# Performance work log

Hardware: AMD Instinct MI355X
Metric: run time of the kernel (lower is better)

Reference implementation:

```python
import jax, jax.numpy as jnp
import numpy as np

B, N_OBJ, OBJ_D = 256, 36, 2048
ATT_D, EMB_D, DEC_D, VOCAB, T = 1024, 1024, 1024, 10000, 20


def setup_inputs() -> dict:
    key = jax.random.key(0)
    ks = jax.random.split(key, 16)
    s = lambda *d: 1.0 / np.sqrt(d[-1])
    inp = {
        'encoder_out': jax.random.normal(ks[0], (B, EMB_D), jnp.float32),
        'objects': jax.random.normal(ks[1], (B, N_OBJ, OBJ_D), jnp.float32),
        'encoded_captions': jax.random.randint(ks[2], (B, T), 0, VOCAB),
        'caption_lengths': jax.random.randint(ks[3], (B, 1), 1, T + 1),
        'emb_table': jax.random.normal(ks[4], (VOCAB, EMB_D), jnp.float32) * 0.02,
        'W_enc_att': jax.random.normal(ks[5], (ATT_D, OBJ_D), jnp.float32) * s(OBJ_D),
        'b_enc_att': jnp.zeros((ATT_D,), jnp.float32),
        'W_dec_att': jax.random.normal(ks[6], (ATT_D, DEC_D), jnp.float32) * s(DEC_D),
        'b_dec_att': jnp.zeros((ATT_D,), jnp.float32),
        'w_full_att': jax.random.normal(ks[7], (1, ATT_D), jnp.float32) * s(ATT_D),
        'b_full_att': jnp.zeros((1,), jnp.float32),
        'W_fbeta': jax.random.normal(ks[8], (OBJ_D, DEC_D), jnp.float32) * s(DEC_D),
        'b_fbeta': jnp.zeros((OBJ_D,), jnp.float32),
        'W_ih': jax.random.normal(ks[9], (4 * DEC_D, EMB_D + OBJ_D), jnp.float32) * s(EMB_D + OBJ_D),
        'W_hh': jax.random.normal(ks[10], (4 * DEC_D, DEC_D), jnp.float32) * s(DEC_D),
        'b_ih': jnp.zeros((4 * DEC_D,), jnp.float32),
        'b_hh': jnp.zeros((4 * DEC_D,), jnp.float32),
        'W_fc': jax.random.normal(ks[11], (VOCAB, DEC_D), jnp.float32) * s(DEC_D),
        'b_fc': jnp.zeros((VOCAB,), jnp.float32),
    }
    return inp


def reference(encoder_out, objects, encoded_captions, caption_lengths,
              emb_table, W_enc_att, b_enc_att, W_dec_att, b_dec_att,
              w_full_att, b_full_att, W_fbeta, b_fbeta,
              W_ih, W_hh, b_ih, b_hh, W_fc, b_fc):
    lengths = caption_lengths[:, 0]
    sort_ind = jnp.argsort(-lengths)  # descending
    lengths = lengths[sort_ind]
    encoder_out = encoder_out[sort_ind]
    objects = objects[sort_ind]
    encoded_captions = encoded_captions[sort_ind]

    embeddings = emb_table[encoded_captions]  # (B, T, E)
    # step t input: encoder_out at t=0, embeddings[:, t-1] afterwards
    step_x = jnp.concatenate([encoder_out[:, None, :], embeddings[:, : T - 1, :]], axis=1)  # (B,T,E)

    att1 = jnp.einsum('bno,ao->bna', objects, W_enc_att) + b_enc_att  # (B,N,A), h-independent

    def step(carry, xs):
        h, c = carry
        x_t, t = xs  # (B,E), scalar
        active = (t < lengths)[:, None]  # (B,1) -- batch_size_t masking (lengths sorted desc)
        att2 = h @ W_dec_att.T + b_dec_att  # (B,A)
        e = (jax.nn.relu(att1 + att2[:, None, :]) @ w_full_att[0] + b_full_att[0])  # (B,N)
        alpha = jax.nn.softmax(e, axis=1)
        awe = jnp.einsum('bn,bno->bo', alpha, objects)  # (B,O)
        gate = jax.nn.sigmoid(h @ W_fbeta.T + b_fbeta)
        awe = gate * awe
        gates = jnp.concatenate([x_t, awe], axis=-1) @ W_ih.T + b_ih + h @ W_hh.T + b_hh
        i, f, g, o = jnp.split(gates, 4, axis=-1)  # torch LSTMCell order
        c_new = jax.nn.sigmoid(f) * c + jax.nn.sigmoid(i) * jnp.tanh(g)
        h_new = jax.nn.sigmoid(o) * jnp.tanh(c_new)
        h = jnp.where(active, h_new, h)
        c = jnp.where(active, c_new, c)
        preds = h_new @ W_fc.T + b_fc  # dropout in eval mode = identity
        preds = jnp.where(active, preds, 0.0)
        alpha = jnp.where(active, alpha, 0.0)
        return (h, c), (preds, alpha)

    h0 = jnp.zeros((B, DEC_D), objects.dtype)
    c0 = jnp.zeros((B, DEC_D), objects.dtype)
    xs = (jnp.swapaxes(step_x, 0, 1), jnp.arange(T))
    _, (preds, alphas) = jax.lax.scan(step, (h0, c0), xs)
    predictions = jnp.swapaxes(preds, 0, 1)  # (B,T,V)
    alphas = jnp.swapaxes(alphas, 0, 1)      # (B,T,N)
    return predictions, encoded_captions, lengths, alphas, sort_ind
```

## Files before the change

kernel.cpp:

```cpp
#include <hip/hip_runtime.h>
#include <hip/hip_bf16.h>
#include <cstdint>
#include <cstddef>

#define BB 256
#define TT 20
#define NOBJ 36
#define OBJD 2048
#define ATTD 1024
#define DECD 1024
#define VOCAB 10000
#define NBIG  17168
#define NBIGP 17280
#define NSPLIT 7168

typedef unsigned short u16;
typedef __attribute__((ext_vector_type(8))) short short8v;
typedef __attribute__((ext_vector_type(4))) float float4v;

__device__ inline u16 f2bf(float f) {
    __hip_bfloat16 h = __float2bfloat16(f);
    return *reinterpret_cast<u16*>(&h);
}
__device__ inline float bu(u16 u) {
    union { unsigned int i; float f; } x;
    x.i = ((unsigned int)u) << 16;
    return x.f;
}
__device__ inline float sigf(float x) { return 1.f / (1.f + expf(-x)); }

__device__ inline void gload16(const u16* g, u16* l) {
    __builtin_amdgcn_global_load_lds(
        (const __attribute__((address_space(1))) unsigned int*)g,
        (__attribute__((address_space(3))) unsigned int*)l, 16, 0, 0);
}

__global__ __launch_bounds__(256) void sort_kernel(
    const int* __restrict__ lens, int* __restrict__ sidx, int* __restrict__ slen,
    int* __restrict__ cnt, float* __restrict__ out_len, float* __restrict__ out_sind)
{
    __shared__ int L[BB];
    __shared__ int SL[BB];
    const int i = threadIdx.x;
    const int li = lens[i];
    L[i] = li;
    __syncthreads();
    int r = 0;
    for (int j = 0; j < BB; ++j) {
        const int lj = L[j];
        if (lj > li || (lj == li && j < i)) r++;
    }
    sidx[r] = i;
    slen[r] = li;
    SL[r] = li;
    out_sind[r] = (float)i;
    out_len[r]  = (float)li;
    __syncthreads();
    if (i < TT) {
        int cc = 0;
        for (int b = 0; b < BB; ++b) cc += (SL[b] > i);
        cnt[i] = cc;
    }
}

__global__ __launch_bounds__(256) void meta_kernel(
    const int* __restrict__ caps, const int* __restrict__ sidx,
    float* __restrict__ out_caps)
{
    const int idx = blockIdx.x * 256 + threadIdx.x;
    const int p = idx / TT, t = idx % TT;
    out_caps[idx] = (float)caps[sidx[p] * TT + t];
}

__global__ __launch_bounds__(256) void gather_objs(
    const float* __restrict__ objs, const int* __restrict__ sidx,
    u16* __restrict__ objsb)
{
    const int row = blockIdx.x;
    const int b = row / NOBJ, n = row - b * NOBJ;
    const float* src = objs + ((size_t)sidx[b] * NOBJ + n) * OBJD;
    u16* dst = objsb + (size_t)row * OBJD;
    const int tid = threadIdx.x;
    #pragma unroll
    for (int j = 0; j < 2; ++j) {
        float4 v = ((const float4*)src)[tid + 256 * j];
        ushort4 s;
        s.x = f2bf(v.x); s.y = f2bf(v.y); s.z = f2bf(v.z); s.w = f2bf(v.w);
        ((ushort4*)dst)[tid + 256 * j] = s;
    }
}

__global__ __launch_bounds__(256) void convWbig(
    const float* __restrict__ Wda, const float* __restrict__ bda,
    const float* __restrict__ Wfb, const float* __restrict__ bfb,
    const float* __restrict__ Whh,
    const float* __restrict__ Wfc, const float* __restrict__ bfc,
    u16* __restrict__ Wb, float* __restrict__ bcat)
{
    const int n = blockIdx.x;
    const int tid = threadIdx.x;
    const float* src = nullptr;
    float bb = 0.f;
    if (n < 1024)        { src = Wda + (size_t)n * 1024;            bb = bda[n]; }
    else if (n < 3072)   { src = Wfb + (size_t)(n - 1024) * 1024;   bb = bfb[n - 1024]; }
    else if (n < 7168)   { src = Whh + (size_t)(n - 3072) * 1024;   bb = 0.f; }
    else if (n < NBIG)   { src = Wfc + (size_t)(n - 7168) * 1024;   bb = bfc[n - 7168]; }
    u16* dst = Wb + (size_t)n * 1024;
    ushort4 s;
    if (src) {
        float4 v = ((const float4*)src)[tid];
        s.x = f2bf(v.x); s.y = f2bf(v.y); s.z = f2bf(v.z); s.w = f2bf(v.w);
    } else { s.x = s.y = s.z = s.w = 0; }
    ((ushort4*)dst)[tid] = s;
    if (tid == 0) bcat[n] = bb;
}

__global__ __launch_bounds__(256) void convWih(
    const float* __restrict__ Wih, const float* __restrict__ bih,
    const float* __restrict__ bhh, u16* __restrict__ Wb, float* __restrict__ bsum)
{
    const int n = blockIdx.x;
    const int tid = threadIdx.x;
    const float* src = Wih + (size_t)n * 3072;
    u16* dst = Wb + (size_t)n * 3072;
    #pragma unroll
    for (int j = 0; j < 3; ++j) {
        float4 v = ((const float4*)src)[tid + 256 * j];
        ushort4 s;
        s.x = f2bf(v.x); s.y = f2bf(v.y); s.z = f2bf(v.z); s.w = f2bf(v.w);
        ((ushort4*)dst)[tid + 256 * j] = s;
    }
    if (tid == 0) bsum[n] = bih[n] + bhh[n];
}

__global__ __launch_bounds__(256) void convWea(
    const float* __restrict__ Wea, u16* __restrict__ Wb)
{
    const int n = blockIdx.x;
    const int tid = threadIdx.x;
    const float* src = Wea + (size_t)n * OBJD;
    u16* dst = Wb + (size_t)n * OBJD;
    #pragma unroll
    for (int j = 0; j < 2; ++j) {
        float4 v = ((const float4*)src)[tid + 256 * j];
        ushort4 s;
        s.x = f2bf(v.x); s.y = f2bf(v.y); s.z = f2bf(v.z); s.w = f2bf(v.w);
        ((ushort4*)dst)[tid + 256 * j] = s;
    }
}

__global__ __launch_bounds__(256) void embed_kernel(
    const float* __restrict__ enc, const int* __restrict__ caps,
    const float* __restrict__ emb, const int* __restrict__ sidx,
    u16* __restrict__ Xb)
{
    const int blk = blockIdx.x;
    const int t = blk >> 8;
    const int b = blk & 255;
    const int sb = sidx[b];
    const float* src = (t == 0) ? (enc + (size_t)sb * DECD)
                                : (emb + (size_t)caps[sb * TT + (t - 1)] * DECD);
    const int tid = threadIdx.x;
    float4 v = ((const float4*)src)[tid];
    ushort4 s;
    s.x = f2bf(v.x); s.y = f2bf(v.y); s.z = f2bf(v.z); s.w = f2bf(v.w);
    ((ushort4*)(Xb + (size_t)blk * DECD))[tid] = s;
}

__global__ __launch_bounds__(256) void zero_hc(float* __restrict__ h, float* __restrict__ c)
{
    const int idx = blockIdx.x * 256 + threadIdx.x;
    if (idx < BB * DECD) h[idx] = 0.f;
    else                 c[idx - BB * DECD] = 0.f;
}

__global__ __launch_bounds__(256) void hcat0_kernel(
    const float* __restrict__ bcat, float* __restrict__ Hcat)
{
    const int col4 = blockIdx.x * 256 + threadIdx.x;
    const int m = blockIdx.y;
    ((float4*)(Hcat + (size_t)m * 7168))[col4] = ((const float4*)bcat)[col4];
}

__global__ __launch_bounds__(256) void gemm128(
    const u16* __restrict__ A, int lda,
    const u16* __restrict__ B, int ldb,
    const float* __restrict__ bias,
    float* __restrict__ Cf, u16* __restrict__ Cb, int ldc,
    int Nreal, int kzlen, size_t zCstride, int pairM,
    int nsplit, float* __restrict__ C2, int ldc2, const int* __restrict__ cntp)
{
    __shared__ u16 As[3][128 * 32];
    __shared__ u16 Bs[3][128 * 32];
    const int tid = threadIdx.x;
    const int lane = tid & 63;
    const int w = tid >> 6;
    const int wr = w >> 1, wc = w & 1;
    int nIdx, mIdx;
    if (pairM) { nIdx = blockIdx.x >> 1; mIdx = blockIdx.x & 1; }
    else       { nIdx = blockIdx.x;      mIdx = blockIdx.y; }
    const int m0 = mIdx * 128;
    const int n0 = nIdx * 128;
    const int kbase = blockIdx.z * kzlen;
    A += kbase;
    B += kbase;
    if (Cf) Cf += (size_t)blockIdx.z * zCstride;

    const int act = cntp ? *cntp : (1 << 30);
    float4v acc[4][4];
    #pragma unroll
    for (int i = 0; i < 4; ++i)
        #pragma unroll
        for (int j = 0; j < 4; ++j) acc[i][j] = (float4v){0.f, 0.f, 0.f, 0.f};

    if (m0 < act) {
        const int r0 = (w * 2 + 0) * 16 + (lane >> 2);
        const int r1 = (w * 2 + 1) * 16 + (lane >> 2);
        const int s0 = (lane & 3) ^ ((r0 >> 1) & 3);
        const int s1 = (lane & 3) ^ ((r1 >> 1) & 3);
        const u16* gA0 = A + (size_t)(m0 + r0) * lda + s0 * 8;
        const u16* gA1 = A + (size_t)(m0 + r1) * lda + s1 * 8;
        const u16* gB0 = B + (size_t)(n0 + r0) * ldb + s0 * 8;
        const u16* gB1 = B + (size_t)(n0 + r1) * ldb + s1 * 8;
        const int la0 = (w * 2 + 0) * 16 * 32;
        const int la1 = (w * 2 + 1) * 16 * 32;

        int ia[4], ib[4];
        #pragma unroll
        for (int mi = 0; mi < 4; ++mi) {
            const int r = wr * 64 + mi * 16 + (lane & 15);
            ia[mi] = r * 32 + (((lane >> 4) ^ ((r >> 1) & 3)) << 3);
        }
        #pragma unroll
        for (int nj = 0; nj < 4; ++nj) {
            const int r = wc * 64 + nj * 16 + (lane & 15);
            ib[nj] = r * 32 + (((lane >> 4) ^ ((r >> 1) & 3)) << 3);
        }

        const int nk = kzlen >> 5;
        #pragma unroll
        for (int p = 0; p < 3; ++p) {
            if (p < nk) {
                const int ko = p * 32;
                gload16(gA0 + ko, &As[p][la0]);
                gload16(gA1 + ko, &As[p][la1]);
                gload16(gB0 + ko, &Bs[p][la0]);
                gload16(gB1 + ko, &Bs[p][la1]);
            }
        }
        int cur = 0;
        for (int it = 0; it < nk; ++it) {
            const int rem = nk - 1 - it;
            if (rem >= 2)      asm volatile("s_waitcnt vmcnt(8)" ::: "memory");
            else if (rem == 1) asm volatile("s_waitcnt vmcnt(4)" ::: "memory");
            else               asm volatile("s_waitcnt vmcnt(0)" ::: "memory");
            __builtin_amdgcn_s_barrier();
            short8v av[4], bv[4];
            #pragma unroll
            for (int mi = 0; mi < 4; ++mi) av[mi] = *(const short8v*)&As[cur][ia[mi]];
            #pragma unroll
            for (int nj = 0; nj < 4; ++nj) bv[nj] = *(const short8v*)&Bs[cur][ib[nj]];
            __builtin_amdgcn_s_setprio(1);
            #pragma unroll
            for (int mi = 0; mi < 4; ++mi)
                #pragma unroll
                for (int nj = 0; nj < 4; ++nj)
                    acc[mi][nj] = __builtin_amdgcn_mfma_f32_16x16x32_bf16(
                        av[mi], bv[nj], acc[mi][nj], 0, 0, 0);
            __builtin_amdgcn_s_setprio(0);
            __builtin_amdgcn_s_barrier();
            if (it + 3 < nk) {
                const int ko = (it + 3) * 32;
                gload16(gA0 + ko, &As[cur][la0]);
                gload16(gA1 + ko, &As[cur][la1]);
                gload16(gB0 + ko, &Bs[cur][la0]);
                gload16(gB1 + ko, &Bs[cur][la1]);
            }
            cur = (cur == 2) ? 0 : cur + 1;
        }
    }

    #pragma unroll
    for (int mi = 0; mi < 4; ++mi) {
        const int mbase = m0 + wr * 64 + mi * 16 + ((lane >> 4) << 2);
        #pragma unroll
        for (int nj = 0; nj < 4; ++nj) {
            const int n = n0 + wc * 64 + nj * 16 + (lane & 15);
            if (n >= Nreal) continue;
            const float bval = bias ? bias[n] : 0.f;
            #pragma unroll
            for (int r = 0; r < 4; ++r) {
                const int m = mbase + r;
                const float v = acc[mi][nj][r] + bval;
                if (n < nsplit) {
                    if (Cb) Cb[(size_t)m * ldc + n] = f2bf(v);
                    else    Cf[(size_t)m * ldc + n] = v;
                } else {
                    C2[(size_t)m * ldc2 + (n - nsplit)] = (m < act) ? v : 0.f;
                }
            }
        }
    }
}

__global__ __launch_bounds__(256) void attn_kernel(
    const u16* __restrict__ att1b, const float* __restrict__ Hcat,
    const u16* __restrict__ objsb,
    const float* __restrict__ wfa, const float* __restrict__ bfa,
    const int* __restrict__ slen, int t,
    float* __restrict__ out_alph, u16* __restrict__ aweb)
{
    const int b = blockIdx.x, z = blockIdx.y, tid = threadIdx.x;
    const bool active = t < slen[b];
    if (!active) {
        if (z == 0 && tid < NOBJ)
            out_alph[((size_t)b * TT + t) * NOBJ + tid] = 0.f;
        return;
    }
    __shared__ float wred[4][40];
    __shared__ float es[40];
    __shared__ float alph[40];
    const int lane = tid & 63, w = tid >> 6;
    const float* hrow = Hcat + (size_t)b * 7168;
    const float4 h4 = ((const float4*)hrow)[tid];
    const float4 w4 = ((const float4*)wfa)[tid];
    const u16* a1base = att1b + (size_t)b * NOBJ * ATTD;

    float ep[NOBJ];
    #pragma unroll
    for (int n = 0; n < NOBJ; ++n) {
        ushort4 a4 = ((const ushort4*)(a1base + (size_t)n * ATTD))[tid];
        const float v0 = fmaxf(bu(a4.x) + h4.x, 0.f);
        const float v1 = fmaxf(bu(a4.y) + h4.y, 0.f);
        const float v2 = fmaxf(bu(a4.z) + h4.z, 0.f);
        const float v3 = fmaxf(bu(a4.w) + h4.w, 0.f);
        ep[n] = v0 * w4.x + v1 * w4.y + v2 * w4.z + v3 * w4.w;
    }
    #pragma unroll
    for (int n = 0; n < NOBJ; ++n) {
        float p = ep[n];
        #pragma unroll
        for (int off = 32; off > 0; off >>= 1) p += __shfl_down(p, off, 64);
        if (lane == 0) wred[w][n] = p;
    }
    __syncthreads();
    if (tid < NOBJ)
        es[tid] = wred[0][tid] + wred[1][tid] + wred[2][tid] + wred[3][tid] + bfa[0];
    __syncthreads();
    if (tid < 64) {
        float mv = (tid < NOBJ) ? es[tid] : -1e30f;
        #pragma unroll
        for (int off = 32; off > 0; off >>= 1) mv = fmaxf(mv, __shfl_xor(mv, off, 64));
        float e = (tid < NOBJ) ? expf(es[tid] - mv) : 0.f;
        float s = e;
        #pragma unroll
        for (int off = 32; off > 0; off >>= 1) s += __shfl_xor(s, off, 64);
        if (tid < NOBJ) alph[tid] = e / s;
    }
    __syncthreads();
    if (z == 0 && tid < NOBJ)
        out_alph[((size_t)b * TT + t) * NOBJ + tid] = alph[tid];

    float acc[4] = {0.f, 0.f, 0.f, 0.f};
    const u16* ob = objsb + (size_t)b * NOBJ * OBJD + z * 1024 + tid * 4;
    #pragma unroll 4
    for (int n = 0; n < NOBJ; ++n) {
        const ushort4 ov = *(const ushort4*)(ob + (size_t)n * OBJD);
        const float al = alph[n];
        acc[0] = fmaf(al, bu(ov.x), acc[0]);
        acc[1] = fmaf(al, bu(ov.y), acc[1]);
        acc[2] = fmaf(al, bu(ov.z), acc[2]);
        acc[3] = fmaf(al, bu(ov.w), acc[3]);
    }
    const float4 g0 = *(const float4*)(hrow + 1024 + z * 1024 + tid * 4);
    ushort4 st;
    st.x = f2bf(acc[0] * sigf(g0.x));
    st.y = f2bf(acc[1] * sigf(g0.y));
    st.z = f2bf(acc[2] * sigf(g0.z));
    st.w = f2bf(acc[3] * sigf(g0.w));
    *(ushort4*)&aweb[(size_t)b * 2048 + z * 1024 + tid * 4] = st;
}

__global__ __launch_bounds__(256) void lstm_kernel(
    const float* __restrict__ G2p, const u16* __restrict__ Gxb,
    const float* __restrict__ Hcat,
    float* __restrict__ h, float* __restrict__ c, u16* __restrict__ hb,
    const int* __restrict__ slen, int t)
{
    const int idx = blockIdx.x * 256 + threadIdx.x;
    const int b = idx >> 8, d4 = idx & 255;
    if (t >= slen[b]) return;
    const float4* pw = (const float4*)(Hcat + (size_t)b * 7168 + 3072);
    const u16* gx = Gxb + ((size_t)(t * BB + b)) * 4096;

    float4 g[4];
    #pragma unroll
    for (int q = 0; q < 4; ++q) {
        const ushort4 xv = ((const ushort4*)(gx + q * 1024))[d4];
        float4 s;
        s.x = bu(xv.x); s.y = bu(xv.y); s.z = bu(xv.z); s.w = bu(xv.w);
        const float4 hv = pw[q * 256 + d4];
        s.x += hv.x; s.y += hv.y; s.z += hv.z; s.w += hv.w;
        #pragma unroll
        for (int p = 0; p < 4; ++p) {
            const float4 pv = ((const float4*)G2p)[(size_t)p * (BB * 1024) + b * 1024 + q * 256 + d4];
            s.x += pv.x; s.y += pv.y; s.z += pv.z; s.w += pv.w;
        }
        g[q] = s;
    }
    float4* hp = (float4*)(h + (size_t)b * 1024);
    float4* cp = (float4*)(c + (size_t)b * 1024);
    const float4 cold = cp[d4];
    float4 cn, hn;
    {
        const float si = sigf(g[0].x), sf = sigf(g[1].x), so = sigf(g[3].x);
        cn.x = sf * cold.x + si * tanhf(g[2].x); hn.x = so * tanhf(cn.x);
    }
    {
        const float si = sigf(g[0].y), sf = sigf(g[1].y), so = sigf(g[3].y);
        cn.y = sf * cold.y + si * tanhf(g[2].y); hn.y = so * tanhf(cn.y);
    }
    {
        const float si = sigf(g[0].z), sf = sigf(g[1].z), so = sigf(g[3].z);
        cn.z = sf * cold.z + si * tanhf(g[2].z); hn.z = so * tanhf(cn.z);
    }
    {
        const float si = sigf(g[0].w), sf = sigf(g[1].w), so = sigf(g[3].w);
        cn.w = sf * cold.w + si * tanhf(g[2].w); hn.w = so * tanhf(cn.w);
    }
    hp[d4] = hn;
    cp[d4] = cn;
    ushort4 s;
    s.x = f2bf(hn.x); s.y = f2bf(hn.y); s.z = f2bf(hn.z); s.w = f2bf(hn.w);
    ((ushort4*)(hb + (size_t)b * 1024))[d4] = s;
}

extern "C" void kernel_launch(void* const* d_in, const int* in_sizes, int n_in,
                              void* d_out, int out_size, void* d_ws, size_t ws_size,
                              hipStream_t stream)
{
    const float* enc  = (const float*)d_in[0];
    const float* objs = (const float*)d_in[1];
    const int*   caps = (const int*)d_in[2];
    const int*   clen = (const int*)d_in[3];
    const float* emb  = (const float*)d_in[4];
    const float* Wea  = (const float*)d_in[5];
    const float* bea  = (const float*)d_in[6];
    const float* Wda  = (const float*)d_in[7];
    const float* bda  = (const float*)d_in[8];
    const float* wfa  = (const float*)d_in[9];
    const float* bfa  = (const float*)d_in[10];
    const float* Wfb  = (const float*)d_in[11];
    const float* bfb  = (const float*)d_in[12];
    const float* Wih  = (const float*)d_in[13];
    const float* Whh  = (const float*)d_in[14];
    const float* bih  = (const float*)d_in[15];
    const float* bhh  = (const float*)d_in[16];
    const float* Wfc  = (const float*)d_in[17];
    const float* bfc  = (const float*)d_in[18];

    float* outP     = (float*)d_out;
    float* out_caps = outP + (size_t)BB * TT * VOCAB;
    float* out_len  = out_caps + BB * TT;
    float* out_alph = out_len + BB;
    float* out_sind = out_alph + (size_t)BB * TT * NOBJ;

    char* wp = (char*)d_ws;
    auto alloc = [&](size_t bytes) -> void* {
        void* r = (void*)wp;
        wp += (bytes + 255) & ~(size_t)255;
        return r;
    };
    int*   sidx  = (int*)alloc(BB * 4);
    int*   slen  = (int*)alloc(BB * 4);
    int*   cnt   = (int*)alloc(32 * 4);
    u16*   objsb = (u16*)alloc((size_t)BB * NOBJ * OBJD * 2);
    u16*   Wbigb = (u16*)alloc((size_t)NBIGP * 1024 * 2);
    float* bcat  = (float*)alloc(NBIGP * 4);
    u16*   Wihb  = (u16*)alloc((size_t)4096 * 3072 * 2);
    float* bsum  = (float*)alloc(4096 * 4);
    u16*   Weab  = (u16*)alloc((size_t)1024 * OBJD * 2);
    u16*   att1b = (u16*)alloc((size_t)BB * NOBJ * ATTD * 2);
    u16*   Xb    = (u16*)alloc((size_t)TT * BB * DECD * 2);
    u16*   Gxb   = (u16*)alloc((size_t)TT * BB * 4096 * 2);
    float* Hcat  = (float*)alloc((size_t)BB * 7168 * 4);
    u16*   aweb  = (u16*)alloc((size_t)BB * 2048 * 2);
    float* G2p   = (float*)alloc((size_t)4 * BB * 4096 * 4);
    float* h     = (float*)alloc((size_t)BB * DECD * 4);
    float* c     = (float*)alloc((size_t)BB * DECD * 4);
    u16*   hb    = (u16*)alloc((size_t)BB * DECD * 2);
    (void)ws_size; (void)in_sizes; (void)n_in; (void)out_size;

    sort_kernel<<<1, 256, 0, stream>>>(clen, sidx, slen, cnt, out_len, out_sind);
    meta_kernel<<<20, 256, 0, stream>>>(caps, sidx, out_caps);
    gather_objs<<<BB * NOBJ, 256, 0, stream>>>(objs, sidx, objsb);
    convWbig<<<NBIGP, 256, 0, stream>>>(Wda, bda, Wfb, bfb, Whh, Wfc, bfc, Wbigb, bcat);
    convWih<<<4096, 256, 0, stream>>>(Wih, bih, bhh, Wihb, bsum);
    convWea<<<1024, 256, 0, stream>>>(Wea, Weab);
    embed_kernel<<<TT * BB, 256, 0, stream>>>(enc, caps, emb, sidx, Xb);
    zero_hc<<<2048, 256, 0, stream>>>(h, c);
    hcat0_kernel<<<dim3(7, 256), 256, 0, stream>>>(bcat, Hcat);

    gemm128<<<dim3(8, 72, 1), 256, 0, stream>>>(
        objsb, OBJD, Weab, OBJD, bea, nullptr, att1b, ATTD,
        ATTD, OBJD, 0, 0, 1 << 30, nullptr, 0, nullptr);

    gemm128<<<dim3(32, 40, 1), 256, 0, stream>>>(
        Xb, DECD, Wihb, 3072, bsum, nullptr, Gxb, 4096,
        4096, DECD, 0, 0, 1 << 30, nullptr, 0, nullptr);

    for (int t = 0; t < TT; ++t) {
        attn_kernel<<<dim3(BB, 2), 256, 0, stream>>>(
            att1b, Hcat, objsb, wfa, bfa, slen, t, out_alph, aweb);
        gemm128<<<dim3(64, 1, 4), 256, 0, stream>>>(
            aweb, 2048, Wihb + 1024, 3072, nullptr, G2p, nullptr, 4096,
            4096, 512, (size_t)BB * 4096, 1, 1 << 30, nullptr, 0, cnt + t);
        lstm_kernel<<<256, 256, 0, stream>>>(G2p, Gxb, Hcat, h, c, hb, slen, t);
        gemm128<<<dim3(NBIGP / 64, 1, 1), 256, 0, stream>>>(
            hb, DECD, Wbigb, DECD, bcat, Hcat, nullptr, 7168,
            NBIG, DECD, 0, 1, NSPLIT, outP + (size_t)t * VOCAB, TT * VOCAB, cnt + t);
    }
}
```

Before: 1.704 ms.

## Fuse all stages into one persistent megakernel with software grid barriers

Replaces the separate preprocessing, GEMM, attention and LSTM launches with a single persistent kernel of 256 blocks that steps through the phases and synchronises them with an atomic grid barrier. The goal is to remove the many per-timestep kernel launches and the idle gaps between them. GEMM tiles are now handed out as a job loop. Only the M tiles needed for the active batch rows are scheduled, and the attention job processes the full 2048-wide object row per block. The trade-off is one block per CU for the heavy prologue GEMMs, which may lower latency hiding, plus barrier spin costs and the risk of deadlock if not all blocks are co-resident.

```diff
diff --git a/kernel.cpp b/kernel.cpp
--- a/kernel.cpp
+++ b/kernel.cpp
@@ -13,6 +13,7 @@
 #define NBIG  17168
 #define NBIGP 17280
 #define NSPLIT 7168
+#define NGRID 256
 
 typedef unsigned short u16;
 typedef __attribute__((ext_vector_type(8))) short short8v;
@@ -35,185 +36,60 @@
         (__attribute__((address_space(3))) unsigned int*)l, 16, 0, 0);
 }
 
-__global__ __launch_bounds__(256) void sort_kernel(
-    const int* __restrict__ lens, int* __restrict__ sidx, int* __restrict__ slen,
-    int* __restrict__ cnt, float* __restrict__ out_len, float* __restrict__ out_sind)
-{
-    __shared__ int L[BB];
-    __shared__ int SL[BB];
-    const int i = threadIdx.x;
-    const int li = lens[i];
-    L[i] = li;
+struct MegaParams {
+    const float* enc; const float* objs; const int* caps; const int* clen;
+    const float* emb;
+    const float* Wea; const float* bea; const float* Wda; const float* bda;
+    const float* wfa; const float* bfa; const float* Wfb; const float* bfb;
+    const float* Wih; const float* Whh; const float* bih; const float* bhh;
+    const float* Wfc; const float* bfc;
+    float* outP; float* out_caps; float* out_len; float* out_alph; float* out_sind;
+    int* bar; int* sidx; int* slen; int* cnt;
+    u16* objsb; u16* Wbigb; float* bcat; u16* Wihb; float* bsum; u16* Weab;
+    u16* att1b; u16* Xb; u16* Gxb; float* Hcat; u16* aweb; float* G2p;
+    float* h; float* c; u16* hb;
+};
+
+__device__ inline void grid_bar(int* bar) {
     __syncthreads();
-    int r = 0;
-    for (int j = 0; j < BB; ++j) {
-        const int lj = L[j];
-        if (lj > li || (lj == li && j < i)) r++;
-    }
-    sidx[r] = i;
-    slen[r] = li;
-    SL[r] = li;
-    out_sind[r] = (float)i;
-    out_len[r]  = (float)li;
+    if (threadIdx.x == 0) {
+        __threadfence();
+        const int gen = __hip_atomic_load(&bar[1], __ATOMIC_RELAXED, __HIP_MEMORY_SCOPE_AGENT);
+        const int prev = __hip_atomic_fetch_add(&bar[0], 1, __ATOMIC_ACQ_REL, __HIP_MEMORY_SCOPE_AGENT);
+        if (prev == NGRID - 1) {
+            __hip_atomic_store(&bar[0], 0, __ATOMIC_RELAXED, __HIP_MEMORY_SCOPE_AGENT);
+            __hip_atomic_store(&bar[1], gen + 1, __ATOMIC_RELEASE, __HIP_MEMORY_SCOPE_AGENT);
+        } else {
+            while (__hip_atomic_load(&bar[1], __ATOMIC_RELAXED, __HIP_MEMORY_SCOPE_AGENT) == gen) {
+                __builtin_amdgcn_s_sleep(1);
+            }
+        }
+        __threadfence();
+    }
     __syncthreads();
-    if (i < TT) {
-        int cc = 0;
-        for (int b = 0; b < BB; ++b) cc += (SL[b] > i);
-        cnt[i] = cc;
-    }
-}
-
-__global__ __launch_bounds__(256) void meta_kernel(
-    const int* __restrict__ caps, const int* __restrict__ sidx,
-    float* __restrict__ out_caps)
-{
-    const int idx = blockIdx.x * 256 + threadIdx.x;
-    const int p = idx / TT, t = idx % TT;
-    out_caps[idx] = (float)caps[sidx[p] * TT + t];
-}
-
-__global__ __launch_bounds__(256) void gather_objs(
-    const float* __restrict__ objs, const int* __restrict__ sidx,
-    u16* __restrict__ objsb)
-{
-    const int row = blockIdx.x;
-    const int b = row / NOBJ, n = row - b * NOBJ;
-    const float* src = objs + ((size_t)sidx[b] * NOBJ + n) * OBJD;
-    u16* dst = objsb + (size_t)row * OBJD;
-    const int tid = threadIdx.x;
-    #pragma unroll
-    for (int j = 0; j < 2; ++j) {
-        float4 v = ((const float4*)src)[tid + 256 * j];
-        ushort4 s;
-        s.x = f2bf(v.x); s.y = f2bf(v.y); s.z = f2bf(v.z); s.w = f2bf(v.w);
-        ((ushort4*)dst)[tid + 256 * j] = s;
-    }
-}
-
-__global__ __launch_bounds__(256) void convWbig(
-    const float* __restrict__ Wda, const float* __restrict__ bda,
-    const float* __restrict__ Wfb, const float* __restrict__ bfb,
-    const float* __restrict__ Whh,
-    const float* __restrict__ Wfc, const float* __restrict__ bfc,
-    u16* __restrict__ Wb, float* __restrict__ bcat)
-{
-    const int n = blockIdx.x;
-    const int tid = threadIdx.x;
-    const float* src = nullptr;
-    float bb = 0.f;
-    if (n < 1024)        { src = Wda + (size_t)n * 1024;            bb = bda[n]; }
-    else if (n < 3072)   { src = Wfb + (size_t)(n - 1024) * 1024;   bb = bfb[n - 1024]; }
-    else if (n < 7168)   { src = Whh + (size_t)(n - 3072) * 1024;   bb = 0.f; }
-    else if (n < NBIG)   { src = Wfc + (size_t)(n - 7168) * 1024;   bb = bfc[n - 7168]; }
-    u16* dst = Wb + (size_t)n * 1024;
-    ushort4 s;
-    if (src) {
-        float4 v = ((const float4*)src)[tid];
-        s.x = f2bf(v.x); s.y = f2bf(v.y); s.z = f2bf(v.z); s.w = f2bf(v.w);
-    } else { s.x = s.y = s.z = s.w = 0; }
-    ((ushort4*)dst)[tid] = s;
-    if (tid == 0) bcat[n] = bb;
-}
-
-__global__ __launch_bounds__(256) void convWih(
-    const float* __restrict__ Wih, const float* __restrict__ bih,
-    const float* __restrict__ bhh, u16* __restrict__ Wb, float* __restrict__ bsum)
-{
-    const int n = blockIdx.x;
-    const int tid = threadIdx.x;
-    const float* src = Wih + (size_t)n * 3072;
-    u16* dst = Wb + (size_t)n * 3072;
-    #pragma unroll
-    for (int j = 0; j < 3; ++j) {
-        float4 v = ((const float4*)src)[tid + 256 * j];
-        ushort4 s;
-        s.x = f2bf(v.x); s.y = f2bf(v.y); s.z = f2bf(v.z); s.w = f2bf(v.w);
-        ((ushort4*)dst)[tid + 256 * j] = s;
-    }
-    if (tid == 0) bsum[n] = bih[n] + bhh[n];
-}
-
-__global__ __launch_bounds__(256) void convWea(
-    const float* __restrict__ Wea, u16* __restrict__ Wb)
-{
-    const int n = blockIdx.x;
-    const int tid = threadIdx.x;
-    const float* src = Wea + (size_t)n * OBJD;
-    u16* dst = Wb + (size_t)n * OBJD;
-    #pragma unroll
-    for (int j = 0; j < 2; ++j) {
-        float4 v = ((const float4*)src)[tid + 256 * j];
-        ushort4 s;
-        s.x = f2bf(v.x); s.y = f2bf(v.y); s.z = f2bf(v.z); s.w = f2bf(v.w);
-        ((ushort4*)dst)[tid + 256 * j] = s;
-    }
-}
-
-__global__ __launch_bounds__(256) void embed_kernel(
-    const float* __restrict__ enc, const int* __restrict__ caps,
-    const float* __restrict__ emb, const int* __restrict__ sidx,
-    u16* __restrict__ Xb)
-{
-    const int blk = blockIdx.x;
-    const int t = blk >> 8;
-    const int b = blk & 255;
-    const int sb = sidx[b];
-    const float* src = (t == 0) ? (enc + (size_t)sb * DECD)
-                                : (emb + (size_t)caps[sb * TT + (t - 1)] * DECD);
-    const int tid = threadIdx.x;
-    float4 v = ((const float4*)src)[tid];
-    ushort4 s;
-    s.x = f2bf(v.x); s.y = f2bf(v.y); s.z = f2bf(v.z); s.w = f2bf(v.w);
-    ((ushort4*)(Xb + (size_t)blk * DECD))[tid] = s;
-}
-
-__global__ __launch_bounds__(256) void zero_hc(float* __restrict__ h, float* __restrict__ c)
-{
-    const int idx = blockIdx.x * 256 + threadIdx.x;
-    if (idx < BB * DECD) h[idx] = 0.f;
-    else                 c[idx - BB * DECD] = 0.f;
-}
-
-__global__ __launch_bounds__(256) void hcat0_kernel(
-    const float* __restrict__ bcat, float* __restrict__ Hcat)
-{
-    const int col4 = blockIdx.x * 256 + threadIdx.x;
-    const int m = blockIdx.y;
-    ((float4*)(Hcat + (size_t)m * 7168))[col4] = ((const float4*)bcat)[col4];
-}
-
-__global__ __launch_bounds__(256) void gemm128(
+}
+
+__device__ void gemm_job(
+    u16* AsB, u16* BsB,
     const u16* __restrict__ A, int lda,
     const u16* __restrict__ B, int ldb,
     const float* __restrict__ bias,
-    float* __restrict__ Cf, u16* __restrict__ Cb, int ldc,
-    int Nreal, int kzlen, size_t zCstride, int pairM,
-    int nsplit, float* __restrict__ C2, int ldc2, const int* __restrict__ cntp)
+    float* Cf, u16* Cb, int ldc,
+    int Nreal, int K, int m0, int n0,
+    int nsplit, float* C2, int ldc2, int act)
 {
-    __shared__ u16 As[3][128 * 32];
-    __shared__ u16 Bs[3][128 * 32];
     const int tid = threadIdx.x;
     const int lane = tid & 63;
     const int w = tid >> 6;
     const int wr = w >> 1, wc = w & 1;
-    int nIdx, mIdx;
-    if (pairM) { nIdx = blockIdx.x >> 1; mIdx = blockIdx.x & 1; }
-    else       { nIdx = blockIdx.x;      mIdx = blockIdx.y; }
-    const int m0 = mIdx * 128;
-    const int n0 = nIdx * 128;
-    const int kbase = blockIdx.z * kzlen;
-    A += kbase;
-    B += kbase;
-    if (Cf) Cf += (size_t)blockIdx.z * zCstride;
-
-    const int act = cntp ? *cntp : (1 << 30);
+
     float4v acc[4][4];
     #pragma unroll
     for (int i = 0; i < 4; ++i)
         #pragma unroll
         for (int j = 0; j < 4; ++j) acc[i][j] = (float4v){0.f, 0.f, 0.f, 0.f};
 
-    if (m0 < act) {
+    {
         const int r0 = (w * 2 + 0) * 16 + (lane >> 2);
         const int r1 = (w * 2 + 1) * 16 + (lane >> 2);
         const int s0 = (lane & 3) ^ ((r0 >> 1) & 3);
@@ -222,8 +98,8 @@
         const u16* gA1 = A + (size_t)(m0 + r1) * lda + s1 * 8;
         const u16* gB0 = B + (size_t)(n0 + r0) * ldb + s0 * 8;
         const u16* gB1 = B + (size_t)(n0 + r1) * ldb + s1 * 8;
-        const int la0 = (w * 2 + 0) * 16 * 32;
-        const int la1 = (w * 2 + 1) * 16 * 32;
+        const int la0 = (w * 2 + 0) * 512;
+        const int la1 = (w * 2 + 1) * 512;
 
         int ia[4], ib[4];
         #pragma unroll
@@ -237,16 +113,14 @@
             ib[nj] = r * 32 + (((lane >> 4) ^ ((r >> 1) & 3)) << 3);
         }
 
-        const int nk = kzlen >> 5;
+        const int nk = K >> 5;
         #pragma unroll
         for (int p = 0; p < 3; ++p) {
-            if (p < nk) {
-                const int ko = p * 32;
-                gload16(gA0 + ko, &As[p][la0]);
-                gload16(gA1 + ko, &As[p][la1]);
-                gload16(gB0 + ko, &Bs[p][la0]);
-                gload16(gB1 + ko, &Bs[p][la1]);
-            }
+            const int ko = p * 32;
+            gload16(gA0 + ko, AsB + p * 4096 + la0);
+            gload16(gA1 + ko, AsB + p * 4096 + la1);
+            gload16(gB0 + ko, BsB + p * 4096 + la0);
+            gload16(gB1 + ko, BsB + p * 4096 + la1);
         }
         int cur = 0;
         for (int it = 0; it < nk; ++it) {
@@ -255,11 +129,13 @@
             else if (rem == 1) asm volatile("s_waitcnt vmcnt(4)" ::: "memory");
             else               asm volatile("s_waitcnt vmcnt(0)" ::: "memory");
             __builtin_amdgcn_s_barrier();
+            const u16* Asc = AsB + cur * 4096;
+            const u16* Bsc = BsB + cur * 4096;
             short8v av[4], bv[4];
             #pragma unroll
-            for (int mi = 0; mi < 4; ++mi) av[mi] = *(const short8v*)&As[cur][ia[mi]];
+            for (int mi = 0; mi < 4; ++mi) av[mi] = *(const short8v*)&Asc[ia[mi]];
             #pragma unroll
-            for (int nj = 0; nj < 4; ++nj) bv[nj] = *(const short8v*)&Bs[cur][ib[nj]];
+            for (int nj = 0; nj < 4; ++nj) bv[nj] = *(const short8v*)&Bsc[ib[nj]];
             __builtin_amdgcn_s_setprio(1);
             #pragma unroll
             for (int mi = 0; mi < 4; ++mi)
@@ -271,10 +147,12 @@
             __builtin_amdgcn_s_barrier();
             if (it + 3 < nk) {
                 const int ko = (it + 3) * 32;
-                gload16(gA0 + ko, &As[cur][la0]);
-                gload16(gA1 + ko, &As[cur][la1]);
-                gload16(gB0 + ko, &Bs[cur][la0]);
-                gload16(gB1 + ko, &Bs[cur][la1]);
+                u16* Asw = AsB + cur * 4096;
+                u16* Bsw = BsB + cur * 4096;
+                gload16(gA0 + ko, Asw + la0);
+                gload16(gA1 + ko, Asw + la1);
+                gload16(gB0 + ko, Bsw + la0);
+                gload16(gB1 + ko, Bsw + la1);
             }
             cur = (cur == 2) ? 0 : cur + 1;
         }
@@ -295,36 +173,24 @@
                 if (n < nsplit) {
                     if (Cb) Cb[(size_t)m * ldc + n] = f2bf(v);
                     else    Cf[(size_t)m * ldc + n] = v;
-                } else {
-                    C2[(size_t)m * ldc2 + (n - nsplit)] = (m < act) ? v : 0.f;
+                } else if (m < act) {
+                    C2[(size_t)m * ldc2 + (n - nsplit)] = v;
                 }
             }
         }
     }
 }
 
-__global__ __launch_bounds__(256) void attn_kernel(
-    const u16* __restrict__ att1b, const float* __restrict__ Hcat,
-    const u16* __restrict__ objsb,
-    const float* __restrict__ wfa, const float* __restrict__ bfa,
-    const int* __restrict__ slen, int t,
-    float* __restrict__ out_alph, u16* __restrict__ aweb)
+__device__ void attn_job(const MegaParams& P, int b, int t,
+                         float (*wred)[40], float* es, float* alph)
 {
-    const int b = blockIdx.x, z = blockIdx.y, tid = threadIdx.x;
-    const bool active = t < slen[b];
-    if (!active) {
-        if (z == 0 && tid < NOBJ)
-            out_alph[((size_t)b * TT + t) * NOBJ + tid] = 0.f;
-        return;
-    }
-    __shared__ float wred[4][40];
-    __shared__ float es[40];
-    __shared__ float alph[40];
+    const int tid = threadIdx.x;
+    if (t >= P.slen[b]) return;
     const int lane = tid & 63, w = tid >> 6;
-    const float* hrow = Hcat + (size_t)b * 7168;
+    const float* hrow = P.Hcat + (size_t)b * 7168;
     const float4 h4 = ((const float4*)hrow)[tid];
-    const float4 w4 = ((const float4*)wfa)[tid];
-    const u16* a1base = att1b + (size_t)b * NOBJ * ATTD;
+    const float4 w4 = ((const float4*)P.wfa)[tid];
+    const u16* a1base = P.att1b + (size_t)b * NOBJ * ATTD;
 
     float ep[NOBJ];
     #pragma unroll
@@ -345,7 +211,7 @@
     }
     __syncthreads();
     if (tid < NOBJ)
-        es[tid] = wred[0][tid] + wred[1][tid] + wred[2][tid] + wred[3][tid] + bfa[0];
+        es[tid] = wred[0][tid] + wred[1][tid] + wred[2][tid] + wred[3][tid] + P.bfa[0];
     __syncthreads();
     if (tid < 64) {
         float mv = (tid < NOBJ) ? es[tid] : -1e30f;
@@ -358,40 +224,35 @@
         if (tid < NOBJ) alph[tid] = e / s;
     }
     __syncthreads();
-    if (z == 0 && tid < NOBJ)
-        out_alph[((size_t)b * TT + t) * NOBJ + tid] = alph[tid];
-
-    float acc[4] = {0.f, 0.f, 0.f, 0.f};
-    const u16* ob = objsb + (size_t)b * NOBJ * OBJD + z * 1024 + tid * 4;
+    if (tid < NOBJ)
+        P.out_alph[((size_t)b * TT + t) * NOBJ + tid] = alph[tid];
+
+    float acc[8] = {0.f, 0.f, 0.f, 0.f, 0.f, 0.f, 0.f, 0.f};
+    const u16* ob = P.objsb + (size_t)b * NOBJ * OBJD + tid * 8;
     #pragma unroll 4
     for (int n = 0; n < NOBJ; ++n) {
-        const ushort4 ov = *(const ushort4*)(ob + (size_t)n * OBJD);
+        const short8v ov = *(const short8v*)(ob + (size_t)n * OBJD);
         const float al = alph[n];
-        acc[0] = fmaf(al, bu(ov.x), acc[0]);
-        acc[1] = fmaf(al, bu(ov.y), acc[1]);
-        acc[2] = fmaf(al, bu(ov.z), acc[2]);
-        acc[3] = fmaf(al, bu(ov.w), acc[3]);
-    }
-    const float4 g0 = *(const float4*)(hrow + 1024 + z * 1024 + tid * 4);
-    ushort4 st;
-    st.x = f2bf(acc[0] * sigf(g0.x));
-    st.y = f2bf(acc[1] * sigf(g0.y));
-    st.z = f2bf(acc[2] * sigf(g0.z));
-    st.w = f2bf(acc[3] * sigf(g0.w));
-    *(ushort4*)&aweb[(size_t)b * 2048 + z * 1024 + tid * 4] = st;
-}
-
-__global__ __launch_bounds__(256) void lstm_kernel(
-    const float* __restrict__ G2p, const u16* __restrict__ Gxb,
-    const float* __restrict__ Hcat,
-    float* __restrict__ h, float* __restrict__ c, u16* __restrict__ hb,
-    const int* __restrict__ slen, int t)
+        #pragma unroll
+        for (int j = 0; j < 8; ++j) acc[j] = fmaf(al, bu((u16)ov[j]), acc[j]);
+    }
+    const float* gp = hrow + 1024 + tid * 8;
+    const float4 g0 = *(const float4*)gp;
+    const float4 g1 = *(const float4*)(gp + 4);
+    const float gt[8] = {sigf(g0.x), sigf(g0.y), sigf(g0.z), sigf(g0.w),
+                         sigf(g1.x), sigf(g1.y), sigf(g1.z), sigf(g1.w)};
+    short8v st;
+    #pragma unroll
+    for (int j = 0; j < 8; ++j) st[j] = (short)f2bf(acc[j] * gt[j]);
+    *(short8v*)&P.aweb[(size_t)b * 2048 + tid * 8] = st;
+}
+
+__device__ void lstm_job(const MegaParams& P, int b, int t)
 {
-    const int idx = blockIdx.x * 256 + threadIdx.x;
-    const int b = idx >> 8, d4 = idx & 255;
-    if (t >= slen[b]) return;
-    const float4* pw = (const float4*)(Hcat + (size_t)b * 7168 + 3072);
-    const u16* gx = Gxb + ((size_t)(t * BB + b)) * 4096;
+    if (t >= P.slen[b]) return;
+    const int d4 = threadIdx.x;
+    const float4* pw = (const float4*)(P.Hcat + (size_t)b * 7168 + 3072);
+    const u16* gx = P.Gxb + ((size_t)(t * BB + b)) * 4096;
 
     float4 g[4];
     #pragma unroll
@@ -403,13 +264,13 @@
         s.x += hv.x; s.y += hv.y; s.z += hv.z; s.w += hv.w;
         #pragma unroll
         for (int p = 0; p < 4; ++p) {
-            const float4 pv = ((const float4*)G2p)[(size_t)p * (BB * 1024) + b * 1024 + q * 256 + d4];
+            const float4 pv = ((const float4*)P.G2p)[(size_t)p * (BB * 1024) + b * 1024 + q * 256 + d4];
             s.x += pv.x; s.y += pv.y; s.z += pv.z; s.w += pv.w;
         }
         g[q] = s;
     }
-    float4* hp = (float4*)(h + (size_t)b * 1024);
-    float4* cp = (float4*)(c + (size_t)b * 1024);
+    float4* hp = (float4*)(P.h + (size_t)b * 1024);
+    float4* cp = (float4*)(P.c + (size_t)b * 1024);
     const float4 cold = cp[d4];
     float4 cn, hn;
     {
@@ -432,38 +293,201 @@
     cp[d4] = cn;
     ushort4 s;
     s.x = f2bf(hn.x); s.y = f2bf(hn.y); s.z = f2bf(hn.z); s.w = f2bf(hn.w);
-    ((ushort4*)(hb + (size_t)b * 1024))[d4] = s;
+    ((ushort4*)(P.hb + (size_t)b * 1024))[d4] = s;
+}
+
+__global__ __launch_bounds__(256) void mega(MegaParams P)
+{
+    __shared__ u16 ldsA[3 * 4096];
+    __shared__ u16 ldsB[3 * 4096];
+    __shared__ float wred[4][40];
+    __shared__ float es[40];
+    __shared__ float alph[40];
+    __shared__ int Ls[BB];
+    __shared__ int SLs[BB];
+    const int bid = blockIdx.x;
+    const int tid = threadIdx.x;
+
+    if (bid == 0) {
+        const int li = P.clen[tid];
+        Ls[tid] = li;
+        __syncthreads();
+        int r = 0;
+        for (int j = 0; j < BB; ++j) {
+            const int lj = Ls[j];
+            if (lj > li || (lj == li && j < tid)) r++;
+        }
+        P.sidx[r] = tid; P.slen[r] = li; SLs[r] = li;
+        P.out_sind[r] = (float)tid; P.out_len[r] = (float)li;
+        __syncthreads();
+        if (tid < TT) {
+            int cc = 0;
+            for (int b2 = 0; b2 < BB; ++b2) cc += (SLs[b2] > tid);
+            P.cnt[tid] = cc;
+        }
+    }
+    for (int n = bid; n < NBIGP; n += NGRID) {
+        const float* src = nullptr;
+        float bbv = 0.f;
+        if (n < 1024)      { src = P.Wda + (size_t)n * 1024;          bbv = P.bda[n]; }
+        else if (n < 3072) { src = P.Wfb + (size_t)(n - 1024) * 1024; bbv = P.bfb[n - 1024]; }
+        else if (n < 7168) { src = P.Whh + (size_t)(n - 3072) * 1024; }
+        else if (n < NBIG) { src = P.Wfc + (size_t)(n - 7168) * 1024; bbv = P.bfc[n - 7168]; }
+        ushort4 s4;
+        if (src) {
+            float4 v = ((const float4*)src)[tid];
+            s4.x = f2bf(v.x); s4.y = f2bf(v.y); s4.z = f2bf(v.z); s4.w = f2bf(v.w);
+        } else { s4.x = s4.y = s4.z = s4.w = 0; }
+        ((ushort4*)(P.Wbigb + (size_t)n * 1024))[tid] = s4;
+        if (tid == 0) P.bcat[n] = bbv;
+    }
+    for (int n = bid; n < 4096; n += NGRID) {
+        const float* src = P.Wih + (size_t)n * 3072;
+        u16* dst = P.Wihb + (size_t)n * 3072;
+        #pragma unroll
+        for (int j = 0; j < 3; ++j) {
+            float4 v = ((const float4*)src)[tid + 256 * j];
+            ushort4 s4;
+            s4.x = f2bf(v.x); s4.y = f2bf(v.y); s4.z = f2bf(v.z); s4.w = f2bf(v.w);
+            ((ushort4*)dst)[tid + 256 * j] = s4;
+        }
+        if (tid == 0) P.bsum[n] = P.bih[n] + P.bhh[n];
+    }
+    for (int n = bid; n < 1024; n += NGRID) {
+        const float* src = P.Wea + (size_t)n * OBJD;
+        u16* dst = P.Weab + (size_t)n * OBJD;
+        #pragma unroll
+        for (int j = 0; j < 2; ++j) {
+            float4 v = ((const float4*)src)[tid + 256 * j];
+            ushort4 s4;
+            s4.x = f2bf(v.x); s4.y = f2bf(v.y); s4.z = f2bf(v.z); s4.w = f2bf(v.w);
+            ((ushort4*)dst)[tid + 256 * j] = s4;
+        }
+    }
+    {
+        const float4 z4 = make_float4(0.f, 0.f, 0.f, 0.f);
+        ((float4*)(P.h + (size_t)bid * 1024))[tid] = z4;
+        ((float4*)(P.c + (size_t)bid * 1024))[tid] = z4;
+        float4* o4 = (float4*)P.outP;
+        for (size_t i = (size_t)bid * 256 + tid; i < 12800000u; i += NGRID * 256) o4[i] = z4;
+        float4* a4 = (float4*)P.out_alph;
+        for (int i = bid * 256 + tid; i < 46080; i += NGRID * 256) a4[i] = z4;
+    }
+    grid_bar(P.bar);
+
+    for (int row = bid; row < BB * NOBJ; row += NGRID) {
+        const int b = row / NOBJ, n = row - b * NOBJ;
+        const float* src = P.objs + ((size_t)P.sidx[b] * NOBJ + n) * OBJD;
+        u16* dst = P.objsb + (size_t)row * OBJD;
+        #pragma unroll
+        for (int j = 0; j < 2; ++j) {
+            float4 v = ((const float4*)src)[tid + 256 * j];
+            ushort4 s4;
+            s4.x = f2bf(v.x); s4.y = f2bf(v.y); s4.z = f2bf(v.z); s4.w = f2bf(v.w);
+            ((ushort4*)dst)[tid + 256 * j] = s4;
+        }
+    }
+    for (int blk = bid; blk < TT * BB; blk += NGRID) {
+        const int t = blk >> 8, b = blk & 255;
+        const int sb = P.sidx[b];
+        const float* src = (t == 0) ? (P.enc + (size_t)sb * DECD)
+                                    : (P.emb + (size_t)P.caps[sb * TT + (t - 1)] * DECD);
+        float4 v = ((const float4*)src)[tid];
+        ushort4 s4;
+        s4.x = f2bf(v.x); s4.y = f2bf(v.y); s4.z = f2bf(v.z); s4.w = f2bf(v.w);
+        ((ushort4*)(P.Xb + (size_t)blk * DECD))[tid] = s4;
+    }
+    if (bid == 1) {
+        for (int i = tid; i < BB * TT; i += 256) {
+            const int p = i / TT, t = i % TT;
+            P.out_caps[i] = (float)P.caps[P.sidx[p] * TT + t];
+        }
+    }
+    {
+        const float4* src = (const float4*)P.bcat;
+        float4* dst = (float4*)(P.Hcat + (size_t)bid * 7168);
+        for (int i = tid; i < 1792; i += 256) dst[i] = src[i];
+    }
+    grid_bar(P.bar);
+
+    for (int j = bid; j < 576 + 1280; j += NGRID) {
+        if (j < 576) {
+            const int n = j / 72, m = j % 72;
+            gemm_job(ldsA, ldsB, P.objsb, OBJD, P.Weab, OBJD, P.bea,
+                     nullptr, P.att1b, ATTD, ATTD, OBJD, m * 128, n * 128,
+                     1 << 30, nullptr, 0, 1 << 30);
+        } else {
+            const int j2 = j - 576;
+            const int n = j2 / 40, m = j2 % 40;
+            gemm_job(ldsA, ldsB, P.Xb, DECD, P.Wihb, 3072, P.bsum,
+                     nullptr, P.Gxb, 4096, 4096, DECD, m * 128, n * 128,
+                     1 << 30, nullptr, 0, 1 << 30);
+        }
+    }
+    grid_bar(P.bar);
+
+    for (int t = 0; t < TT; ++t) {
+        const int act = P.cnt[t];
+        const int mt = (act > 128) ? 2 : 1;
+
+        attn_job(P, bid, t, wred, es, alph);
+        grid_bar(P.bar);
+
+        for (int j = bid; j < mt * 128; j += NGRID) {
+            const int kz = j & 3, q = j >> 2;
+            const int n = q & 31, m = q >> 5;
+            gemm_job(ldsA, ldsB,
+                     P.aweb + kz * 512, 2048,
+                     P.Wihb + 1024 + kz * 512, 3072,
+                     nullptr, P.G2p + (size_t)kz * (BB * 4096), nullptr, 4096,
+                     4096, 512, m * 128, n * 128, 1 << 30, nullptr, 0, 1 << 30);
+        }
+        grid_bar(P.bar);
+
+        lstm_job(P, bid, t);
+        grid_bar(P.bar);
+
+        for (int j = bid; j < mt * 135; j += NGRID) {
+            int n, m;
+            if (mt == 2) { n = j >> 1; m = j & 1; } else { n = j; m = 0; }
+            gemm_job(ldsA, ldsB, P.hb, DECD, P.Wbigb, DECD, P.bcat,
+                     P.Hcat, nullptr, 7168, NBIG, DECD, m * 128, n * 128,
+                     NSPLIT, P.outP + (size_t)t * VOCAB, TT * VOCAB, act);
+        }
+        grid_bar(P.bar);
+    }
 }
 
 extern "C" void kernel_launch(void* const* d_in, const int* in_sizes, int n_in,
                               void* d_out, int out_size, void* d_ws, size_t ws_size,
                               hipStream_t stream)
 {
-    const float* enc  = (const float*)d_in[0];
-    const float* objs = (const float*)d_in[1];
-    const int*   caps = (const int*)d_in[2];
-    const int*   clen = (const int*)d_in[3];
-    const float* emb  = (const float*)d_in[4];
-    const float* Wea  = (const float*)d_in[5];
-    const float* bea  = (const float*)d_in[6];
-    const float* Wda  = (const float*)d_in[7];
-    const float* bda  = (const float*)d_in[8];
-    const float* wfa  = (const float*)d_in[9];
-    const float* bfa  = (const float*)d_in[10];
-    const float* Wfb  = (const float*)d_in[11];
-    const float* bfb  = (const float*)d_in[12];
-    const float* Wih  = (const float*)d_in[13];
-    const float* Whh  = (const float*)d_in[14];
-    const float* bih  = (const float*)d_in[15];
-    const float* bhh  = (const float*)d_in[16];
-    const float* Wfc  = (const float*)d_in[17];
-    const float* bfc  = (const float*)d_in[18];
-
-    float* outP     = (float*)d_out;
-    float* out_caps = outP + (size_t)BB * TT * VOCAB;
-    float* out_len  = out_caps + BB * TT;
-    float* out_alph = out_len + BB;
-    float* out_sind = out_alph + (size_t)BB * TT * NOBJ;
+    MegaParams P;
+    P.enc  = (const float*)d_in[0];
+    P.objs = (const float*)d_in[1];
+    P.caps = (const int*)d_in[2];
+    P.clen = (const int*)d_in[3];
+    P.emb  = (const float*)d_in[4];
+    P.Wea  = (const float*)d_in[5];
+    P.bea  = (const float*)d_in[6];
+    P.Wda  = (const float*)d_in[7];
+    P.bda  = (const float*)d_in[8];
+    P.wfa  = (const float*)d_in[9];
+    P.bfa  = (const float*)d_in[10];
+    P.Wfb  = (const float*)d_in[11];
+    P.bfb  = (const float*)d_in[12];
+    P.Wih  = (const float*)d_in[13];
+    P.Whh  = (const float*)d_in[14];
+    P.bih  = (const float*)d_in[15];
+    P.bhh  = (const float*)d_in[16];
+    P.Wfc  = (const float*)d_in[17];
+    P.bfc  = (const float*)d_in[18];
+
+    P.outP     = (float*)d_out;
+    P.out_caps = P.outP + (size_t)BB * TT * VOCAB;
+    P.out_len  = P.out_caps + BB * TT;
+    P.out_alph = P.out_len + BB;
+    P.out_sind = P.out_alph + (size_t)BB * TT * NOBJ;
 
     char* wp = (char*)d_ws;
     auto alloc = [&](size_t bytes) -> void* {
@@ -471,53 +495,27 @@
         wp += (bytes + 255) & ~(size_t)255;
         return r;
     };
-    int*   sidx  = (int*)alloc(BB * 4);
-    int*   slen  = (int*)alloc(BB * 4);
-    int*   cnt   = (int*)alloc(32 * 4);
-    u16*   objsb = (u16*)alloc((size_t)BB * NOBJ * OBJD * 2);
-    u16*   Wbigb = (u16*)alloc((size_t)NBIGP * 1024 * 2);
-    float* bcat  = (float*)alloc(NBIGP * 4);
-    u16*   Wihb  = (u16*)alloc((size_t)4096 * 3072 * 2);
-    float* bsum  = (float*)alloc(4096 * 4);
-    u16*   Weab  = (u16*)alloc((size_t)1024 * OBJD * 2);
-    u16*   att1b = (u16*)alloc((size_t)BB * NOBJ * ATTD * 2);
-    u16*   Xb    = (u16*)alloc((size_t)TT * BB * DECD * 2);
-    u16*   Gxb   = (u16*)alloc((size_t)TT * BB * 4096 * 2);
-    float* Hcat  = (float*)alloc((size_t)BB * 7168 * 4);
-    u16*   aweb  = (u16*)alloc((size_t)BB * 2048 * 2);
-    float* G2p   = (float*)alloc((size_t)4 * BB * 4096 * 4);
-    float* h     = (float*)alloc((size_t)BB * DECD * 4);
-    float* c     = (float*)alloc((size_t)BB * DECD * 4);
-    u16*   hb    = (u16*)alloc((size_t)BB * DECD * 2);
+    P.bar   = (int*)alloc(256);
+    P.sidx  = (int*)alloc(BB * 4);
+    P.slen  = (int*)alloc(BB * 4);
+    P.cnt   = (int*)alloc(32 * 4);
+    P.objsb = (u16*)alloc((size_t)BB * NOBJ * OBJD * 2);
+    P.Wbigb = (u16*)alloc((size_t)NBIGP * 1024 * 2);
+    P.bcat  = (float*)alloc(NBIGP * 4);
+    P.Wihb  = (u16*)alloc((size_t)4096 * 3072 * 2);
+    P.bsum  = (float*)alloc(4096 * 4);
+    P.Weab  = (u16*)alloc((size_t)1024 * OBJD * 2);
+    P.att1b = (u16*)alloc((size_t)BB * NOBJ * ATTD * 2);
+    P.Xb    = (u16*)alloc((size_t)TT * BB * DECD * 2);
+    P.Gxb   = (u16*)alloc((size_t)TT * BB * 4096 * 2);
+    P.Hcat  = (float*)alloc((size_t)BB * 7168 * 4);
+    P.aweb  = (u16*)alloc((size_t)BB * 2048 * 2);
+    P.G2p   = (float*)alloc((size_t)4 * BB * 4096 * 4);
+    P.h     = (float*)alloc((size_t)BB * DECD * 4);
+    P.c     = (float*)alloc((size_t)BB * DECD * 4);
+    P.hb    = (u16*)alloc((size_t)BB * DECD * 2);
     (void)ws_size; (void)in_sizes; (void)n_in; (void)out_size;
 
-    sort_kernel<<<1, 256, 0, stream>>>(clen, sidx, slen, cnt, out_len, out_sind);
-    meta_kernel<<<20, 256, 0, stream>>>(caps, sidx, out_caps);
-    gather_objs<<<BB * NOBJ, 256, 0, stream>>>(objs, sidx, objsb);
-    convWbig<<<NBIGP, 256, 0, stream>>>(Wda, bda, Wfb, bfb, Whh, Wfc, bfc, Wbigb, bcat);
-    convWih<<<4096, 256, 0, stream>>>(Wih, bih, bhh, Wihb, bsum);
-    convWea<<<1024, 256, 0, stream>>>(Wea, Weab);
-    embed_kernel<<<TT * BB, 256, 0, stream>>>(enc, caps, emb, sidx, Xb);
-    zero_hc<<<2048, 256, 0, stream>>>(h, c);
-    hcat0_kernel<<<dim3(7, 256), 256, 0, stream>>>(bcat, Hcat);
-
-    gemm128<<<dim3(8, 72, 1), 256, 0, stream>>>(
-        objsb, OBJD, Weab, OBJD, bea, nullptr, att1b, ATTD,
-        ATTD, OBJD, 0, 0, 1 << 30, nullptr, 0, nullptr);
-
-    gemm128<<<dim3(32, 40, 1), 256, 0, stream>>>(
-        Xb, DECD, Wihb, 3072, bsum, nullptr, Gxb, 4096,
-        4096, DECD, 0, 0, 1 << 30, nullptr, 0, nullptr);
-
-    for (int t = 0; t < TT; ++t) {
-        attn_kernel<<<dim3(BB, 2), 256, 0, stream>>>(
-            att1b, Hcat, objsb, wfa, bfa, slen, t, out_alph, aweb);
-        gemm128<<<dim3(64, 1, 4), 256, 0, stream>>>(
-            aweb, 2048, Wihb + 1024, 3072, nullptr, G2p, nullptr, 4096,
-            4096, 512, (size_t)BB * 4096, 1, 1 << 30, nullptr, 0, cnt + t);
-        lstm_kernel<<<256, 256, 0, stream>>>(G2p, Gxb, Hcat, h, c, hb, slen, t);
-        gemm128<<<dim3(NBIGP / 64, 1, 1), 256, 0, stream>>>(
-            hb, DECD, Wbigb, DECD, bcat, Hcat, nullptr, 7168,
-            NBIG, DECD, 0, 1, NSPLIT, outP + (size_t)t * VOCAB, TT * VOCAB, cnt + t);
-    }
-}
+    hipMemsetAsync(P.bar, 0, 256, stream);
+    mega<<<NGRID, 256, 0, stream>>>(P);
+}
```

New measurement: 4.422 ms. 2.6x slower.
